# Kernel optimization log

Measured on AMD Instinct MI355X. Metric: run time of the kernel, lower is better.

## Reference

```python
import jax, jax.numpy as jnp
import numpy as np

TOP_K = 2


def setup_inputs() -> dict:
    key = jax.random.key(0)
    ks = jax.random.split(key, 5)
    B, S, D, E, I = 1, 2048, 2880, 8, 2880
    scale_in = 1.0 / np.sqrt(D)
    scale_mid = 1.0 / np.sqrt(I)
    return {
        "x": jax.random.normal(ks[0], (B, S, D), dtype=jnp.float32),
        "w_router": jax.random.normal(ks[1], (D, E), dtype=jnp.float32) * scale_in,
        "w_gate": jax.random.normal(ks[2], (E, D, I), dtype=jnp.float32) * scale_in,
        "w_up": jax.random.normal(ks[3], (E, D, I), dtype=jnp.float32) * scale_in,
        "w_down": jax.random.normal(ks[4], (E, I, D), dtype=jnp.float32) * scale_mid,
    }


def reference(x, w_router, w_gate, w_up, w_down):
    B, S, D = x.shape
    E = w_router.shape[1]
    t = x.reshape(-1, D)  # [T, D] flattened tokens

    # --- RouterTopK: softmax over experts, then top-k selection ---
    logits = t @ w_router                      # [T, E]
    affinities = jax.nn.softmax(logits, axis=-1)
    top_vals, top_idx = jax.lax.top_k(affinities, TOP_K)   # [T, K]
    # normalize_top_k_affinities=True: renormalize selected weights to sum to 1
    top_vals = top_vals / jnp.sum(top_vals, axis=-1, keepdims=True)

    # scatter normalized weights into dense [T, E] combine matrix
    T = t.shape[0]
    tok = jnp.arange(T)[:, None]
    weights = jnp.zeros((T, E), dtype=t.dtype).at[tok, top_idx].set(top_vals)

    # --- Expert SiLU-GLU MLPs (computed per expert, combined by weights) ---
    gate = jnp.einsum("td,edi->eti", t, w_gate)  # [E, T, I]
    up = jnp.einsum("td,edi->eti", t, w_up)      # [E, T, I]
    h = jax.nn.silu(gate) * up                   # [E, T, I]
    y = jnp.einsum("eti,eid->etd", h, w_down)    # [E, T, D]

    out = jnp.einsum("te,etd->td", weights, y)   # affinity-weighted combine
    return out.reshape(B, S, D)
```

## Files before the change

### kernel.cpp

```cpp
#include <hip/hip_runtime.h>
#include <hip/hip_fp16.h>
#include <stdint.h>
#include <math.h>


typedef _Float16 f16;
typedef _Float16 f16x8 __attribute__((ext_vector_type(8)));
typedef float f32x4 __attribute__((ext_vector_type(4)));

#define T_TOK 2048
#define DDIM 2880
#define NEXP 8
#define IDIM 2880
#define BK 64
#define NKT 45

#define BM_A 128
#define BN1_A 96
#define BN2_A 192
#define MAXMT_A 40
#define NB1_A (30*MAXMT_A)
#define NB2_A (15*MAXMT_A)
#define BM_B 256
#define BN1_B 96
#define BN2_B 192
#define MAXMT_B 24
#define NB1_B (30*MAXMT_B)
#define NB2_B (15*MAXMT_B)

#define SLOT_CAP 6144

#define M_COUNT 0
#define M_CUR 8
#define M_OFFS 16
#define M_NTILES 25
#define M_TILE_E 32
#define M_TILE_R0 96
#define M_SLOT_TOK 160
#define M_SLOT_OF (160+SLOT_CAP)
#define M_TOK_E (M_SLOT_OF + 2*T_TOK)
#define META_INTS (M_TOK_E + 2*T_TOK)

#define WT_B   ((size_t)NEXP*DDIM*IDIM*2)
#define A_WGT  ((size_t)0)
#define A_WUT  (A_WGT + WT_B)
#define A_WDT  A_WGT
#define A_HBUF (A_WUT + WT_B)
#define A_YBUF (A_HBUF + (size_t)5120*IDIM*2)
#define A_XH   (A_YBUF + (size_t)5120*DDIM*2)
#define A_META (A_XH + (size_t)T_TOK*DDIM*2)
#define A_SLOTW (A_META + (size_t)META_INTS*4)
#define A_TOKW  (A_SLOTW + (size_t)SLOT_CAP*4)
#define A_NEED  (A_TOKW + (size_t)T_TOK*2*4)

#define B_HBUF ((size_t)0)
#define B_XH   (B_HBUF + (size_t)SLOT_CAP*IDIM*2)
#define B_YBUF B_XH
#define B_META (B_YBUF + (size_t)SLOT_CAP*DDIM*2)
#define B_SLOTW (B_META + (size_t)META_INTS*4)
#define B_TOKW  (B_SLOTW + (size_t)SLOT_CAP*4)
#define B_NEED  (B_TOKW + (size_t)T_TOK*2*4)

__device__ __forceinline__ int swz(int row) { return ((row ^ (row >> 3)) & 7) << 4; }

__device__ __forceinline__ void gload_lds16(const void* gp, void* lp) {
  __builtin_amdgcn_global_load_lds(
      (const __attribute__((address_space(1))) uint32_t*)gp,
      (__attribute__((address_space(3))) uint32_t*)lp,
      16, 0, 0);
}

__global__ __launch_bounds__(256) void k_router(
    const float* __restrict__ x, const float* __restrict__ wr,
    int* __restrict__ meta, float* __restrict__ tok_w) {
  const int lane = threadIdx.x & 63;
  const int t = blockIdx.x * 4 + (threadIdx.x >> 6);
  double acc[NEXP];
#pragma unroll
  for (int e = 0; e < NEXP; e++) acc[e] = 0.0;
  for (int d = lane; d < DDIM; d += 64) {
    float xv = x[(size_t)t * DDIM + d];
    float4 w0 = *(const float4*)(wr + (size_t)d * NEXP);
    float4 w1 = *(const float4*)(wr + (size_t)d * NEXP + 4);
    acc[0] += (double)xv * (double)w0.x;
    acc[1] += (double)xv * (double)w0.y;
    acc[2] += (double)xv * (double)w0.z;
    acc[3] += (double)xv * (double)w0.w;
    acc[4] += (double)xv * (double)w1.x;
    acc[5] += (double)xv * (double)w1.y;
    acc[6] += (double)xv * (double)w1.z;
    acc[7] += (double)xv * (double)w1.w;
  }
#pragma unroll
  for (int m = 32; m >= 1; m >>= 1) {
#pragma unroll
    for (int e = 0; e < NEXP; e++) acc[e] += __shfl_xor(acc[e], m, 64);
  }
  if (lane == 0) {
    int e0 = 0;
#pragma unroll
    for (int e = 1; e < NEXP; e++) if (acc[e] > acc[e0]) e0 = e;
    int e1 = (e0 == 0) ? 1 : 0;
#pragma unroll
    for (int e = 0; e < NEXP; e++) if (e != e0 && acc[e] > acc[e1]) e1 = e;
    double w0 = 1.0 / (1.0 + exp(acc[e1] - acc[e0]));
    meta[M_TOK_E + 2*t]     = e0;
    meta[M_TOK_E + 2*t + 1] = e1;
    tok_w[2*t]     = (float)w0;
    tok_w[2*t + 1] = (float)(1.0 - w0);
    atomicAdd(&meta[M_COUNT + e0], 1);
    atomicAdd(&meta[M_COUNT + e1], 1);
  }
}

__global__ __launch_bounds__(256) void k_xcvt(const float* __restrict__ x, f16* __restrict__ xh) {
  size_t i = ((size_t)blockIdx.x * 256 + threadIdx.x) * 8;
  float4 a = *(const float4*)(x + i);
  float4 b = *(const float4*)(x + i + 4);
  f16x8 v;
  v[0]=(f16)a.x; v[1]=(f16)a.y; v[2]=(f16)a.z; v[3]=(f16)a.w;
  v[4]=(f16)b.x; v[5]=(f16)b.y; v[6]=(f16)b.z; v[7]=(f16)b.w;
  *(f16x8*)(xh + i) = v;
}

__global__ __launch_bounds__(256) void k_cvt_w(const float* __restrict__ src, f16* __restrict__ dst) {
  __shared__ f16 t[64][72];
  const int tile = blockIdx.x;
  const int e = blockIdx.y;
  const int k0 = (tile / 45) * 64;
  const int i0 = (tile % 45) * 64;
  const int tid = threadIdx.x;
  const float* sp = src + ((size_t)e * DDIM + k0) * IDIM + i0;
#pragma unroll
  for (int p = 0; p < 4; p++) {
    int kr = p * 16 + (tid >> 4);
    int c0 = (tid & 15) * 4;
    float4 v = *(const float4*)(sp + (size_t)kr * IDIM + c0);
    t[c0 + 0][kr] = (f16)v.x;
    t[c0 + 1][kr] = (f16)v.y;
    t[c0 + 2][kr] = (f16)v.z;
    t[c0 + 3][kr] = (f16)v.w;
  }
  __syncthreads();
#pragma unroll
  for (int p = 0; p < 2; p++) {
    int row = tid >> 2;
    int ch = (tid & 3) + p * 4;
    f16x8 o = *(const f16x8*)&t[row][ch * 8];
    *(f16x8*)(dst + ((size_t)e * IDIM + i0 + row) * DDIM + k0 + ch * 8) = o;
  }
}

__global__ __launch_bounds__(64) void k_scan(int* __restrict__ meta, float* __restrict__ slot_w, int bm) {
  __shared__ int s_off[NEXP], s_cnt[NEXP], s_pc[NEXP];
  if (threadIdx.x == 0) {
    int run = 0, nt = 0;
    for (int e = 0; e < NEXP; e++) {
      int c = meta[M_COUNT + e];
      int mt = (c + bm - 1) / bm;
      meta[M_OFFS + e] = run;
      s_off[e] = run; s_cnt[e] = c; s_pc[e] = mt * bm;
      for (int j = 0; j < mt; j++) { meta[M_TILE_E + nt] = e; meta[M_TILE_R0 + nt] = run + j * bm; nt++; }
      run += mt * bm;
      meta[M_CUR + e] = 0;
    }
    meta[M_OFFS + NEXP] = run;
    meta[M_NTILES] = nt;
  }
  __syncthreads();
  for (int e = 0; e < NEXP; e++) {
    for (int i = s_cnt[e] + (int)threadIdx.x; i < s_pc[e]; i += 64) {
      meta[M_SLOT_TOK + s_off[e] + i] = 0;
      slot_w[s_off[e] + i] = 0.0f;
    }
  }
}

__global__ __launch_bounds__(256) void k_scatter(int* __restrict__ meta,
    float* __restrict__ slot_w, const float* __restrict__ tok_w) {
  int t = blockIdx.x * 256 + threadIdx.x;
  if (t >= T_TOK) return;
#pragma unroll
  for (int k = 0; k < 2; k++) {
    int e = meta[M_TOK_E + 2*t + k];
    int pos = atomicAdd(&meta[M_CUR + e], 1);
    int slot = meta[M_OFFS + e] + pos;
    meta[M_SLOT_TOK + slot] = t;
    slot_w[slot] = tok_w[2*t + k];
    meta[M_SLOT_OF + 2*t + k] = slot;
  }
}


__global__ __launch_bounds__(256, 3) void kg1(
    const f16* __restrict__ xh, const f16* __restrict__ wgT, const f16* __restrict__ wuT,
    f16* __restrict__ hbuf, const int* __restrict__ meta) {
  const int id = blockIdx.x;
  const int sid = (id & 7) * (NB1_A / 8) + (id >> 3);
  const int mt = sid % MAXMT_A;
  const int nb = sid / MAXMT_A;
  if (mt >= meta[M_NTILES]) return;
  const int e  = meta[M_TILE_E + mt];
  const int r0 = meta[M_TILE_R0 + mt];
  const int n0 = nb * BN1_A;

  __shared__ ushort sA[BM_A * BK];
  __shared__ ushort sBg[BN1_A * BK];
  __shared__ ushort sBu[BN1_A * BK];

  const int tid = threadIdx.x;
  const int lane = tid & 63;
  const int w = tid >> 6;
  const int wm = w >> 1, wn = w & 1;

  const char* aG[4]; int aL[4];
#pragma unroll
  for (int i = 0; i < 4; i++) {
    int seg = w * 4 + i;
    int row = seg * 8 + (lane >> 3);
    int colb = ((lane & 7) * 16) ^ swz(row);
    int tok = meta[M_SLOT_TOK + r0 + row];
    aG[i] = (const char*)(xh + (size_t)tok * DDIM) + colb;
    aL[i] = seg * 1024;
  }
  const char* gG[3]; const char* uG[3]; int bL[3];
#pragma unroll
  for (int i = 0; i < 3; i++) {
    int seg = w * 3 + i;
    int row = seg * 8 + (lane >> 3);
    int colb = ((lane & 7) * 16) ^ swz(row);
    gG[i] = (const char*)(wgT + ((size_t)e * IDIM + n0 + row) * DDIM) + colb;
    uG[i] = (const char*)(wuT + ((size_t)e * IDIM + n0 + row) * DDIM) + colb;
    bL[i] = seg * 1024;
  }

  f32x4 accG[4][3], accU[4][3];
#pragma unroll
  for (int i = 0; i < 4; i++)
#pragma unroll
    for (int j = 0; j < 3; j++) { accG[i][j] = {0.f,0.f,0.f,0.f}; accU[i][j] = {0.f,0.f,0.f,0.f}; }

  for (int kt = 0; kt < NKT; kt++) {
    __syncthreads();
#pragma unroll
    for (int i = 0; i < 4; i++) gload_lds16(aG[i] + kt * 128, (char*)sA + aL[i]);
#pragma unroll
    for (int i = 0; i < 3; i++) gload_lds16(gG[i] + kt * 128, (char*)sBg + bL[i]);
#pragma unroll
    for (int i = 0; i < 3; i++) gload_lds16(uG[i] + kt * 128, (char*)sBu + bL[i]);
    __syncthreads();
#pragma unroll
    for (int kk = 0; kk < 2; kk++) {
      const int gb = kk * 64 + ((lane >> 4) * 16);
      f16x8 af[4], bg[3], bu[3];
#pragma unroll
      for (int fm = 0; fm < 4; fm++) {
        int row = wm * 64 + fm * 16 + (lane & 15);
        af[fm] = *(const f16x8*)((const char*)sA + row * 128 + (gb ^ swz(row)));
      }
#pragma unroll
      for (int fn = 0; fn < 3; fn++) {
        int row = wn * 48 + fn * 16 + (lane & 15);
        bg[fn] = *(const f16x8*)((const char*)sBg + row * 128 + (gb ^ swz(row)));
        bu[fn] = *(const f16x8*)((const char*)sBu + row * 128 + (gb ^ swz(row)));
      }
#pragma unroll
      for (int fm = 0; fm < 4; fm++)
#pragma unroll
        for (int fn = 0; fn < 3; fn++) {
          accG[fm][fn] = __builtin_amdgcn_mfma_f32_16x16x32_f16(af[fm], bg[fn], accG[fm][fn], 0, 0, 0);
          accU[fm][fn] = __builtin_amdgcn_mfma_f32_16x16x32_f16(af[fm], bu[fn], accU[fm][fn], 0, 0, 0);
        }
    }
  }
  const int rl4 = (lane >> 4) * 4;
  const int cl  = lane & 15;
#pragma unroll
  for (int fm = 0; fm < 4; fm++)
#pragma unroll
    for (int fn = 0; fn < 3; fn++)
#pragma unroll
      for (int j = 0; j < 4; j++) {
        int row = wm * 64 + fm * 16 + rl4 + j;
        int col = n0 + wn * 48 + fn * 16 + cl;
        float g = accG[fm][fn][j], u = accU[fm][fn][j];
        float h = g * u / (1.0f + __expf(-g));
        hbuf[(size_t)(r0 + row) * IDIM + col] = (f16)h;
      }
}

__global__ __launch_bounds__(256, 3) void kg2(
    const f16* __restrict__ hbuf, const f16* __restrict__ wdT,
    f16* __restrict__ ybuf, const int* __restrict__ meta, const float* __restrict__ slot_w) {
  const int id = blockIdx.x;
  const int sid = (id & 7) * (NB2_A / 8) + (id >> 3);
  const int mt = sid % MAXMT_A;
  const int nb = sid / MAXMT_A;
  if (mt >= meta[M_NTILES]) return;
  const int e  = meta[M_TILE_E + mt];
  const int r0 = meta[M_TILE_R0 + mt];
  const int n0 = nb * BN2_A;

  __shared__ ushort sA[BM_A * BK];
  __shared__ ushort sB[BN2_A * BK];

  const int tid = threadIdx.x;
  const int lane = tid & 63;
  const int w = tid >> 6;
  const int wm = w >> 1, wn = w & 1;

  const char* aG[4]; int aL[4];
#pragma unroll
  for (int i = 0; i < 4; i++) {
    int seg = w * 4 + i;
    int row = seg * 8 + (lane >> 3);
    int colb = ((lane & 7) * 16) ^ swz(row);
    aG[i] = (const char*)(hbuf + (size_t)(r0 + row) * IDIM) + colb;
    aL[i] = seg * 1024;
  }
  const char* bG[6]; int bL[6];
#pragma unroll
  for (int i = 0; i < 6; i++) {
    int seg = w * 6 + i;
    int row = seg * 8 + (lane >> 3);
    int colb = ((lane & 7) * 16) ^ swz(row);
    bG[i] = (const char*)(wdT + ((size_t)e * DDIM + n0 + row) * IDIM) + colb;
    bL[i] = seg * 1024;
  }

  f32x4 acc[4][6];
#pragma unroll
  for (int i = 0; i < 4; i++)
#pragma unroll
    for (int j = 0; j < 6; j++) acc[i][j] = {0.f,0.f,0.f,0.f};

  for (int kt = 0; kt < NKT; kt++) {
    __syncthreads();
#pragma unroll
    for (int i = 0; i < 4; i++) gload_lds16(aG[i] + kt * 128, (char*)sA + aL[i]);
#pragma unroll
    for (int i = 0; i < 6; i++) gload_lds16(bG[i] + kt * 128, (char*)sB + bL[i]);
    __syncthreads();
#pragma unroll
    for (int kk = 0; kk < 2; kk++) {
      const int gb = kk * 64 + ((lane >> 4) * 16);
      f16x8 af[4], bf[6];
#pragma unroll
      for (int fm = 0; fm < 4; fm++) {
        int row = wm * 64 + fm * 16 + (lane & 15);
        af[fm] = *(const f16x8*)((const char*)sA + row * 128 + (gb ^ swz(row)));
      }
#pragma unroll
      for (int fn = 0; fn < 6; fn++) {
        int row = wn * 96 + fn * 16 + (lane & 15);
        bf[fn] = *(const f16x8*)((const char*)sB + row * 128 + (gb ^ swz(row)));
      }
#pragma unroll
      for (int fm = 0; fm < 4; fm++)
#pragma unroll
        for (int fn = 0; fn < 6; fn++)
          acc[fm][fn] = __builtin_amdgcn_mfma_f32_16x16x32_f16(af[fm], bf[fn], acc[fm][fn], 0, 0, 0);
    }
  }
  const int rl4 = (lane >> 4) * 4;
  const int cl  = lane & 15;
#pragma unroll
  for (int fm = 0; fm < 4; fm++)
#pragma unroll
    for (int j = 0; j < 4; j++) {
      int row = wm * 64 + fm * 16 + rl4 + j;
      int slot = r0 + row;
      float wv = slot_w[slot];
#pragma unroll
      for (int fn = 0; fn < 6; fn++) {
        int col = n0 + wn * 96 + fn * 16 + cl;
        ybuf[(size_t)slot * DDIM + col] = (f16)(acc[fm][fn][j] * wv);
      }
    }
}

__global__ __launch_bounds__(256) void k_combine(const f16* __restrict__ ybuf,
    const int* __restrict__ meta, float* __restrict__ out) {
  size_t idx = (size_t)blockIdx.x * 256 + threadIdx.x;
  int t = (int)(idx / (DDIM/8));
  int c = (int)(idx % (DDIM/8));
  int s0 = meta[M_SLOT_OF + 2*t];
  int s1 = meta[M_SLOT_OF + 2*t + 1];
  f16x8 a = *(const f16x8*)(ybuf + (size_t)s0 * DDIM + c*8);
  f16x8 b = *(const f16x8*)(ybuf + (size_t)s1 * DDIM + c*8);
  float4 o0, o1;
  o0.x = (float)a[0] + (float)b[0];
  o0.y = (float)a[1] + (float)b[1];
  o0.z = (float)a[2] + (float)b[2];
  o0.w = (float)a[3] + (float)b[3];
  o1.x = (float)a[4] + (float)b[4];
  o1.y = (float)a[5] + (float)b[5];
  o1.z = (float)a[6] + (float)b[6];
  o1.w = (float)a[7] + (float)b[7];
  float* op = out + (size_t)t * DDIM + c*8;
  *(float4*)op = o0;
  *(float4*)(op + 4) = o1;
}


__global__ __launch_bounds__(512, 2) void kg1_fb(
    const f16* __restrict__ xh, const float* __restrict__ wg, const float* __restrict__ wu,
    f16* __restrict__ hbuf, const int* __restrict__ meta) {
  const int id = blockIdx.x;
  const int sid = (id & 7) * (NB1_B / 8) + (id >> 3);
  const int mt = sid % MAXMT_B;
  const int nb = sid / MAXMT_B;
  if (mt >= meta[M_NTILES]) return;
  const int e  = meta[M_TILE_E + mt];
  const int r0 = meta[M_TILE_R0 + mt];
  const int n0 = nb * BN1_B;

  __shared__ ushort sA[2][BM_B * BK];
  __shared__ ushort sB[2][2][BN1_B * BK];

  const int tid  = threadIdx.x;
  const int lane = tid & 63;
  const int w    = tid >> 6;
  const int wm   = w >> 1;
  const int gu   = w & 1;

  const char* a_gbase[4];
  int a_loff[4];
#pragma unroll
  for (int i = 0; i < 4; i++) {
    int seg = w * 4 + i;
    int row = seg * 8 + (lane >> 3);
    int colb = ((lane & 7) * 16) ^ swz(row);
    int tok = meta[M_SLOT_TOK + r0 + row];
    a_gbase[i] = (const char*)(xh + (size_t)tok * DDIM) + colb;
    a_loff[i] = seg * 1024;
  }
  const int bm_ = tid / 192;
  const int tt  = tid % 192;
  const int bn0 = (tt % 24) * 4;
  const int bk0 = (tt / 24) * 8;
  const bool bact = tid < 384;
  const float* bsrc = (bm_ ? wu : wg) + ((size_t)e * DDIM + bk0) * IDIM + n0 + bn0;

  float4 vB[8];
  f32x4 acc[4][6];
#pragma unroll
  for (int i = 0; i < 4; i++)
#pragma unroll
    for (int j = 0; j < 6; j++) acc[i][j] = {0.f,0.f,0.f,0.f};

#pragma unroll
  for (int i = 0; i < 4; i++) gload_lds16(a_gbase[i], (char*)sA[0] + a_loff[i]);
  if (bact) {
#pragma unroll
    for (int j = 0; j < 8; j++) vB[j] = *(const float4*)(bsrc + (size_t)j * IDIM);
#pragma unroll
    for (int c = 0; c < 4; c++) {
      f16x8 p;
#pragma unroll
      for (int j = 0; j < 8; j++) {
        float fc = (c==0) ? vB[j].x : (c==1) ? vB[j].y : (c==2) ? vB[j].z : vB[j].w;
        p[j] = (f16)fc;
      }
      *(f16x8*)((char*)sB[0][bm_] + (bn0 + c) * 128 + ((bk0 * 2) ^ swz(bn0 + c))) = p;
    }
  }
  __syncthreads();

  for (int kt = 0; kt < NKT; kt++) {
    const int cur = kt & 1;
    if (kt + 1 < NKT) {
#pragma unroll
      for (int i = 0; i < 4; i++)
        gload_lds16(a_gbase[i] + (kt + 1) * 128, (char*)sA[cur ^ 1] + a_loff[i]);
      if (bact) {
        const float* bs = bsrc + (size_t)(kt + 1) * BK * IDIM;
#pragma unroll
        for (int j = 0; j < 8; j++) vB[j] = *(const float4*)(bs + (size_t)j * IDIM);
      }
    }
#pragma unroll
    for (int kk = 0; kk < 2; kk++) {
      const int gb = kk * 64 + ((lane >> 4) * 16);
      f16x8 af[4], bf[6];
#pragma unroll
      for (int fm = 0; fm < 4; fm++) {
        int row = wm * 64 + fm * 16 + (lane & 15);
        af[fm] = *(const f16x8*)((const char*)sA[cur] + row * 128 + (gb ^ swz(row)));
      }
#pragma unroll
      for (int fn = 0; fn < 6; fn++) {
        int row = fn * 16 + (lane & 15);
        bf[fn] = *(const f16x8*)((const char*)sB[cur][gu] + row * 128 + (gb ^ swz(row)));
      }
#pragma unroll
      for (int fm = 0; fm < 4; fm++)
#pragma unroll
        for (int fn = 0; fn < 6; fn++)
          acc[fm][fn] = __builtin_amdgcn_mfma_f32_16x16x32_f16(af[fm], bf[fn], acc[fm][fn], 0, 0, 0);
    }
    if (kt + 1 < NKT && bact) {
#pragma unroll
      for (int c = 0; c < 4; c++) {
        f16x8 p;
#pragma unroll
        for (int j = 0; j < 8; j++) {
          float fc = (c==0) ? vB[j].x : (c==1) ? vB[j].y : (c==2) ? vB[j].z : vB[j].w;
          p[j] = (f16)fc;
        }
        *(f16x8*)((char*)sB[cur ^ 1][bm_] + (bn0 + c) * 128 + ((bk0 * 2) ^ swz(bn0 + c))) = p;
      }
    }
    __syncthreads();
  }

  float* u_lds = (float*)&sA[0][0];
  const int rl4 = (lane >> 4) * 4;
  const int cl  = lane & 15;
#pragma unroll
  for (int r = 0; r < 2; r++) {
    __syncthreads();
    if (gu == 1) {
#pragma unroll
      for (int fi = 0; fi < 2; fi++)
#pragma unroll
        for (int fn = 0; fn < 6; fn++)
#pragma unroll
          for (int j = 0; j < 4; j++)
            u_lds[wm * 3200 + (fi * 16 + rl4 + j) * 100 + fn * 16 + cl] = acc[2*r + fi][fn][j];
    }
    __syncthreads();
    if (gu == 0) {
#pragma unroll
      for (int fi = 0; fi < 2; fi++) {
        int fm = 2*r + fi;
#pragma unroll
        for (int fn = 0; fn < 6; fn++)
#pragma unroll
          for (int j = 0; j < 4; j++) {
            float u = u_lds[wm * 3200 + (fi * 16 + rl4 + j) * 100 + fn * 16 + cl];
            float g = acc[fm][fn][j];
            float h = g * u / (1.0f + __expf(-g));
            hbuf[(size_t)(r0 + wm * 64 + fm * 16 + rl4 + j) * IDIM + n0 + fn * 16 + cl] = (f16)h;
          }
      }
    }
  }
}

__global__ __launch_bounds__(512, 2) void kg2_fb(
    const f16* __restrict__ hbuf, const float* __restrict__ wd,
    f16* __restrict__ ybuf, const int* __restrict__ meta, const float* __restrict__ slot_w) {
  const int id = blockIdx.x;
  const int sid = (id & 7) * (NB2_B / 8) + (id >> 3);
  const int mt = sid % MAXMT_B;
  const int nb = sid / MAXMT_B;
  if (mt >= meta[M_NTILES]) return;
  const int e  = meta[M_TILE_E + mt];
  const int r0 = meta[M_TILE_R0 + mt];
  const int n0 = nb * BN2_B;

  __shared__ ushort sA[2][BM_B * BK];
  __shared__ ushort sB1[2][BN2_B * BK];

  const int tid  = threadIdx.x;
  const int lane = tid & 63;
  const int w    = tid >> 6;
  const int wm   = w >> 1;
  const int wn   = w & 1;

  const char* a_gbase[4];
  int a_loff[4];
#pragma unroll
  for (int i = 0; i < 4; i++) {
    int seg = w * 4 + i;
    int row = seg * 8 + (lane >> 3);
    int colb = ((lane & 7) * 16) ^ swz(row);
    a_gbase[i] = (const char*)(hbuf + (size_t)(r0 + row) * IDIM) + colb;
    a_loff[i] = seg * 1024;
  }
  const int half = tid / 192;
  const int tt   = tid % 192;
  const int bn0  = half * 96 + (tt % 24) * 4;
  const int bk0  = (tt / 24) * 8;
  const bool bact = tid < 384;
  const float* bsrc = wd + ((size_t)e * IDIM + bk0) * DDIM + n0 + bn0;

  float4 vB[8];
  f32x4 acc[4][6];
#pragma unroll
  for (int i = 0; i < 4; i++)
#pragma unroll
    for (int j = 0; j < 6; j++) acc[i][j] = {0.f,0.f,0.f,0.f};

#pragma unroll
  for (int i = 0; i < 4; i++) gload_lds16(a_gbase[i], (char*)sA[0] + a_loff[i]);
  if (bact) {
#pragma unroll
    for (int j = 0; j < 8; j++) vB[j] = *(const float4*)(bsrc + (size_t)j * DDIM);
#pragma unroll
    for (int c = 0; c < 4; c++) {
      f16x8 p;
#pragma unroll
      for (int j = 0; j < 8; j++) {
        float fc = (c==0) ? vB[j].x : (c==1) ? vB[j].y : (c==2) ? vB[j].z : vB[j].w;
        p[j] = (f16)fc;
      }
      *(f16x8*)((char*)sB1[0] + (bn0 + c) * 128 + ((bk0 * 2) ^ swz(bn0 + c))) = p;
    }
  }
  __syncthreads();

  for (int kt = 0; kt < NKT; kt++) {
    const int cur = kt & 1;
    if (kt + 1 < NKT) {
#pragma unroll
      for (int i = 0; i < 4; i++)
        gload_lds16(a_gbase[i] + (kt + 1) * 128, (char*)sA[cur ^ 1] + a_loff[i]);
      if (bact) {
        const float* bs = bsrc + (size_t)(kt + 1) * BK * DDIM;
#pragma unroll
        for (int j = 0; j < 8; j++) vB[j] = *(const float4*)(bs + (size_t)j * DDIM);
      }
    }
#pragma unroll
    for (int kk = 0; kk < 2; kk++) {
      const int gb = kk * 64 + ((lane >> 4) * 16);
      f16x8 af[4], bf[6];
#pragma unroll
      for (int fm = 0; fm < 4; fm++) {
        int row = wm * 64 + fm * 16 + (lane & 15);
        af[fm] = *(const f16x8*)((const char*)sA[cur] + row * 128 + (gb ^ swz(row)));
      }
#pragma unroll
      for (int fn = 0; fn < 6; fn++) {
        int row = wn * 96 + fn * 16 + (lane & 15);
        bf[fn] = *(const f16x8*)((const char*)sB1[cur] + row * 128 + (gb ^ swz(row)));
      }
#pragma unroll
      for (int fm = 0; fm < 4; fm++)
#pragma unroll
        for (int fn = 0; fn < 6; fn++)
          acc[fm][fn] = __builtin_amdgcn_mfma_f32_16x16x32_f16(af[fm], bf[fn], acc[fm][fn], 0, 0, 0);
    }
    if (kt + 1 < NKT && bact) {
#pragma unroll
      for (int c = 0; c < 4; c++) {
        f16x8 p;
#pragma unroll
        for (int j = 0; j < 8; j++) {
          float fc = (c==0) ? vB[j].x : (c==1) ? vB[j].y : (c==2) ? vB[j].z : vB[j].w;
          p[j] = (f16)fc;
        }
        *(f16x8*)((char*)sB1[cur ^ 1] + (bn0 + c) * 128 + ((bk0 * 2) ^ swz(bn0 + c))) = p;
      }
    }
    __syncthreads();
  }

  const int rl4 = (lane >> 4) * 4;
  const int cl  = lane & 15;
#pragma unroll
  for (int fm = 0; fm < 4; fm++)
#pragma unroll
    for (int j = 0; j < 4; j++) {
      int row = wm * 64 + fm * 16 + rl4 + j;
      int slot = r0 + row;
      float wv = slot_w[slot];
#pragma unroll
      for (int fn = 0; fn < 6; fn++) {
        int col = n0 + wn * 96 + fn * 16 + cl;
        ybuf[(size_t)slot * DDIM + col] = (f16)(acc[fm][fn][j] * wv);
      }
    }
}

extern "C" void kernel_launch(void* const* d_in, const int* in_sizes, int n_in,
                              void* d_out, int out_size, void* d_ws, size_t ws_size,
                              hipStream_t stream) {
  const float* x  = (const float*)d_in[0];
  const float* wr = (const float*)d_in[1];
  const float* wg = (const float*)d_in[2];
  const float* wu = (const float*)d_in[3];
  const float* wd = (const float*)d_in[4];
  float* out = (float*)d_out;
  char* ws = (char*)d_ws;

  if (ws_size >= A_NEED) {
    f16* wgT = (f16*)(ws + A_WGT);
    f16* wuT = (f16*)(ws + A_WUT);
    f16* wdT = (f16*)(ws + A_WDT);
    f16* hbuf = (f16*)(ws + A_HBUF);
    f16* ybuf = (f16*)(ws + A_YBUF);
    f16* xh   = (f16*)(ws + A_XH);
    int* meta = (int*)(ws + A_META);
    float* slot_w = (float*)(ws + A_SLOTW);
    float* tok_w  = (float*)(ws + A_TOKW);

    hipMemsetAsync(meta + M_COUNT, 0, NEXP * sizeof(int), stream);
    k_cvt_w<<<dim3(2025, NEXP), 256, 0, stream>>>(wg, wgT);
    k_cvt_w<<<dim3(2025, NEXP), 256, 0, stream>>>(wu, wuT);
    k_router<<<T_TOK/4, 256, 0, stream>>>(x, wr, meta, tok_w);
    k_xcvt<<<(T_TOK*DDIM/8)/256, 256, 0, stream>>>(x, xh);
    k_scan<<<1, 64, 0, stream>>>(meta, slot_w, BM_A);
    k_scatter<<<(T_TOK + 255)/256, 256, 0, stream>>>(meta, slot_w, tok_w);
    kg1<<<NB1_A, 256, 0, stream>>>(xh, wgT, wuT, hbuf, meta);
    k_cvt_w<<<dim3(2025, NEXP), 256, 0, stream>>>(wd, wdT);
    kg2<<<NB2_A, 256, 0, stream>>>(hbuf, wdT, ybuf, meta, slot_w);
    k_combine<<<(T_TOK*DDIM/8)/256, 256, 0, stream>>>(ybuf, meta, out);
  } else if (ws_size >= B_NEED) {
    f16* hbuf = (f16*)(ws + B_HBUF);
    f16* xh   = (f16*)(ws + B_XH);
    f16* ybuf = (f16*)(ws + B_YBUF);
    int* meta = (int*)(ws + B_META);
    float* slot_w = (float*)(ws + B_SLOTW);
    float* tok_w  = (float*)(ws + B_TOKW);

    hipMemsetAsync(meta + M_COUNT, 0, NEXP * sizeof(int), stream);
    k_router<<<T_TOK/4, 256, 0, stream>>>(x, wr, meta, tok_w);
    k_xcvt<<<(T_TOK*DDIM/8)/256, 256, 0, stream>>>(x, xh);
    k_scan<<<1, 64, 0, stream>>>(meta, slot_w, BM_B);
    k_scatter<<<(T_TOK + 255)/256, 256, 0, stream>>>(meta, slot_w, tok_w);
    kg1_fb<<<NB1_B, 512, 0, stream>>>(xh, wg, wu, hbuf, meta);
    kg2_fb<<<NB2_B, 512, 0, stream>>>(hbuf, wd, ybuf, meta, slot_w);
    k_combine<<<(T_TOK*DDIM/8)/256, 256, 0, stream>>>(ybuf, meta, out);
  }
}
```

Measured before the change: 691.3 us.

## Fuse prep kernels, overlap down-weight conversion with GEMM1, double-buffer LDS tiles

Merges the gate/up weight conversion, router and x conversion into one persistent launch. When the workspace is large enough, it also folds the down-weight transpose into the GEMM1 launch so the conversion blocks run alongside GEMM1 tiles. The scan and scatter steps become a single block that uses shared-memory atomics. Both GEMM kernels switch to double-buffered LDS prefetch with one barrier per k-step, which raises LDS per block to 80KB and lowers the launch-bounds occupancy hint from 3 to 2.

```diff
diff --git a/kernel.cpp b/kernel.cpp
--- a/kernel.cpp
+++ b/kernel.cpp
@@ -21,6 +21,8 @@
 #define MAXMT_A 40
 #define NB1_A (30*MAXMT_A)
 #define NB2_A (15*MAXMT_A)
+#define NCVT 16200
+
 #define BM_B 256
 #define BN1_B 96
 #define BN2_B 192
@@ -31,7 +33,6 @@
 #define SLOT_CAP 6144
 
 #define M_COUNT 0
-#define M_CUR 8
 #define M_OFFS 16
 #define M_NTILES 25
 #define M_TILE_E 32
@@ -42,24 +43,13 @@
 #define META_INTS (M_TOK_E + 2*T_TOK)
 
 #define WT_B   ((size_t)NEXP*DDIM*IDIM*2)
-#define A_WGT  ((size_t)0)
-#define A_WUT  (A_WGT + WT_B)
-#define A_WDT  A_WGT
-#define A_HBUF (A_WUT + WT_B)
-#define A_YBUF (A_HBUF + (size_t)5120*IDIM*2)
-#define A_XH   (A_YBUF + (size_t)5120*DDIM*2)
-#define A_META (A_XH + (size_t)T_TOK*DDIM*2)
-#define A_SLOTW (A_META + (size_t)META_INTS*4)
-#define A_TOKW  (A_SLOTW + (size_t)SLOT_CAP*4)
-#define A_NEED  (A_TOKW + (size_t)T_TOK*2*4)
-
-#define B_HBUF ((size_t)0)
-#define B_XH   (B_HBUF + (size_t)SLOT_CAP*IDIM*2)
-#define B_YBUF B_XH
-#define B_META (B_YBUF + (size_t)SLOT_CAP*DDIM*2)
-#define B_SLOTW (B_META + (size_t)META_INTS*4)
-#define B_TOKW  (B_SLOTW + (size_t)SLOT_CAP*4)
-#define B_NEED  (B_TOKW + (size_t)T_TOK*2*4)
+#define HB_B   ((size_t)5120*IDIM*2)
+#define XH_B   ((size_t)T_TOK*DDIM*2)
+#define TAIL_B ((size_t)META_INTS*4 + (size_t)SLOT_CAP*4 + (size_t)T_TOK*2*4)
+
+#define A3_NEED (3*WT_B + 2*HB_B + XH_B + TAIL_B)
+#define A2_NEED (2*WT_B + 2*HB_B + XH_B + TAIL_B)
+#define BF_NEED ((size_t)SLOT_CAP*IDIM*2 + (size_t)SLOT_CAP*DDIM*2 + TAIL_B)
 
 __device__ __forceinline__ int swz(int row) { return ((row ^ (row >> 3)) & 7) << 4; }
 
@@ -70,11 +60,40 @@
       16, 0, 0);
 }
 
-__global__ __launch_bounds__(256) void k_router(
-    const float* __restrict__ x, const float* __restrict__ wr,
-    int* __restrict__ meta, float* __restrict__ tok_w) {
-  const int lane = threadIdx.x & 63;
-  const int t = blockIdx.x * 4 + (threadIdx.x >> 6);
+
+__device__ __forceinline__ void cvt_body(const float* __restrict__ src, f16* __restrict__ dst,
+                                          int blk, int tid, char* smem) {
+  f16 (*t)[72] = (f16 (*)[72])smem;
+  const int e = blk / 2025;
+  const int tile = blk % 2025;
+  const int k0 = (tile / 45) * 64;
+  const int i0 = (tile % 45) * 64;
+  const float* sp = src + ((size_t)e * DDIM + k0) * IDIM + i0;
+#pragma unroll
+  for (int p = 0; p < 4; p++) {
+    int kr = p * 16 + (tid >> 4);
+    int c0 = (tid & 15) * 4;
+    float4 v = *(const float4*)(sp + (size_t)kr * IDIM + c0);
+    t[c0 + 0][kr] = (f16)v.x;
+    t[c0 + 1][kr] = (f16)v.y;
+    t[c0 + 2][kr] = (f16)v.z;
+    t[c0 + 3][kr] = (f16)v.w;
+  }
+  __syncthreads();
+#pragma unroll
+  for (int p = 0; p < 2; p++) {
+    int row = tid >> 2;
+    int ch = (tid & 3) + p * 4;
+    f16x8 o = *(const f16x8*)&t[row][ch * 8];
+    *(f16x8*)(dst + ((size_t)e * IDIM + i0 + row) * DDIM + k0 + ch * 8) = o;
+  }
+}
+
+__device__ __forceinline__ void router_body(const float* __restrict__ x, const float* __restrict__ wr,
+                                            int* __restrict__ meta, float* __restrict__ tok_w,
+                                            int blk, int tid) {
+  const int lane = tid & 63;
+  const int t = blk * 4 + (tid >> 6);
   double acc[NEXP];
 #pragma unroll
   for (int e = 0; e < NEXP; e++) acc[e] = 0.0;
@@ -113,8 +132,9 @@
   }
 }
 
-__global__ __launch_bounds__(256) void k_xcvt(const float* __restrict__ x, f16* __restrict__ xh) {
-  size_t i = ((size_t)blockIdx.x * 256 + threadIdx.x) * 8;
+__device__ __forceinline__ void xcvt_body(const float* __restrict__ x, f16* __restrict__ xh,
+                                          int blk, int tid) {
+  size_t i = ((size_t)blk * 256 + tid) * 8;
   float4 a = *(const float4*)(x + i);
   float4 b = *(const float4*)(x + i + 4);
   f16x8 v;
@@ -123,79 +143,74 @@
   *(f16x8*)(xh + i) = v;
 }
 
-__global__ __launch_bounds__(256) void k_cvt_w(const float* __restrict__ src, f16* __restrict__ dst) {
-  __shared__ f16 t[64][72];
-  const int tile = blockIdx.x;
-  const int e = blockIdx.y;
-  const int k0 = (tile / 45) * 64;
-  const int i0 = (tile % 45) * 64;
+__global__ __launch_bounds__(256) void k_p1(
+    const float* __restrict__ x, const float* __restrict__ wr,
+    const float* __restrict__ wg, const float* __restrict__ wu,
+    f16* __restrict__ wgT, f16* __restrict__ wuT, f16* __restrict__ xh,
+    int* __restrict__ meta, float* __restrict__ tok_w) {
+  __shared__ char smem[9216];
+  int b = blockIdx.x;
   const int tid = threadIdx.x;
-  const float* sp = src + ((size_t)e * DDIM + k0) * IDIM + i0;
-#pragma unroll
-  for (int p = 0; p < 4; p++) {
-    int kr = p * 16 + (tid >> 4);
-    int c0 = (tid & 15) * 4;
-    float4 v = *(const float4*)(sp + (size_t)kr * IDIM + c0);
-    t[c0 + 0][kr] = (f16)v.x;
-    t[c0 + 1][kr] = (f16)v.y;
-    t[c0 + 2][kr] = (f16)v.z;
-    t[c0 + 3][kr] = (f16)v.w;
-  }
-  __syncthreads();
-#pragma unroll
-  for (int p = 0; p < 2; p++) {
-    int row = tid >> 2;
-    int ch = (tid & 3) + p * 4;
-    f16x8 o = *(const f16x8*)&t[row][ch * 8];
-    *(f16x8*)(dst + ((size_t)e * IDIM + i0 + row) * DDIM + k0 + ch * 8) = o;
-  }
-}
-
-__global__ __launch_bounds__(64) void k_scan(int* __restrict__ meta, float* __restrict__ slot_w, int bm) {
-  __shared__ int s_off[NEXP], s_cnt[NEXP], s_pc[NEXP];
-  if (threadIdx.x == 0) {
+  if (b < NCVT) { cvt_body(wg, wgT, b, tid, smem); return; }
+  b -= NCVT;
+  if (b < NCVT) { cvt_body(wu, wuT, b, tid, smem); return; }
+  b -= NCVT;
+  if (b < T_TOK/4) { router_body(x, wr, meta, tok_w, b, tid); return; }
+  b -= T_TOK/4;
+  xcvt_body(x, xh, b, tid);
+}
+
+__global__ __launch_bounds__(256) void k_router(const float* x, const float* wr, int* meta, float* tok_w) {
+  router_body(x, wr, meta, tok_w, blockIdx.x, threadIdx.x);
+}
+__global__ __launch_bounds__(256) void k_xcvt(const float* x, f16* xh) {
+  xcvt_body(x, xh, blockIdx.x, threadIdx.x);
+}
+__global__ __launch_bounds__(256) void k_cvt_w(const float* src, f16* dst) {
+  __shared__ char smem[9216];
+  cvt_body(src, dst, blockIdx.x, threadIdx.x, smem);
+}
+
+__global__ __launch_bounds__(256) void k_scan_scatter(
+    int* __restrict__ meta, float* __restrict__ slot_w, const float* __restrict__ tok_w, int bm) {
+  __shared__ int s_off[NEXP], s_cnt[NEXP], s_pc[NEXP], s_cur[NEXP];
+  const int tid = threadIdx.x;
+  if (tid == 0) {
     int run = 0, nt = 0;
     for (int e = 0; e < NEXP; e++) {
       int c = meta[M_COUNT + e];
       int mt = (c + bm - 1) / bm;
       meta[M_OFFS + e] = run;
-      s_off[e] = run; s_cnt[e] = c; s_pc[e] = mt * bm;
+      s_off[e] = run; s_cnt[e] = c; s_pc[e] = mt * bm; s_cur[e] = 0;
       for (int j = 0; j < mt; j++) { meta[M_TILE_E + nt] = e; meta[M_TILE_R0 + nt] = run + j * bm; nt++; }
       run += mt * bm;
-      meta[M_CUR + e] = 0;
     }
     meta[M_OFFS + NEXP] = run;
     meta[M_NTILES] = nt;
   }
   __syncthreads();
   for (int e = 0; e < NEXP; e++) {
-    for (int i = s_cnt[e] + (int)threadIdx.x; i < s_pc[e]; i += 64) {
+    for (int i = s_cnt[e] + tid; i < s_pc[e]; i += 256) {
       meta[M_SLOT_TOK + s_off[e] + i] = 0;
       slot_w[s_off[e] + i] = 0.0f;
     }
   }
-}
-
-__global__ __launch_bounds__(256) void k_scatter(int* __restrict__ meta,
-    float* __restrict__ slot_w, const float* __restrict__ tok_w) {
-  int t = blockIdx.x * 256 + threadIdx.x;
-  if (t >= T_TOK) return;
-#pragma unroll
-  for (int k = 0; k < 2; k++) {
-    int e = meta[M_TOK_E + 2*t + k];
-    int pos = atomicAdd(&meta[M_CUR + e], 1);
-    int slot = meta[M_OFFS + e] + pos;
-    meta[M_SLOT_TOK + slot] = t;
-    slot_w[slot] = tok_w[2*t + k];
-    meta[M_SLOT_OF + 2*t + k] = slot;
-  }
-}
-
-
-__global__ __launch_bounds__(256, 3) void kg1(
+  for (int t = tid; t < T_TOK; t += 256) {
+#pragma unroll
+    for (int k = 0; k < 2; k++) {
+      int e = meta[M_TOK_E + 2*t + k];
+      int pos = atomicAdd(&s_cur[e], 1);
+      int slot = s_off[e] + pos;
+      meta[M_SLOT_TOK + slot] = t;
+      slot_w[slot] = tok_w[2*t + k];
+      meta[M_SLOT_OF + 2*t + k] = slot;
+    }
+  }
+}
+
+__device__ __forceinline__ void kg1_body(
     const f16* __restrict__ xh, const f16* __restrict__ wgT, const f16* __restrict__ wuT,
-    f16* __restrict__ hbuf, const int* __restrict__ meta) {
-  const int id = blockIdx.x;
+    f16* __restrict__ hbuf, const int* __restrict__ meta, int id, int tid, char* smem) {
   const int sid = (id & 7) * (NB1_A / 8) + (id >> 3);
   const int mt = sid % MAXMT_A;
   const int nb = sid / MAXMT_A;
@@ -204,11 +219,6 @@
   const int r0 = meta[M_TILE_R0 + mt];
   const int n0 = nb * BN1_A;
 
-  __shared__ ushort sA[BM_A * BK];
-  __shared__ ushort sBg[BN1_A * BK];
-  __shared__ ushort sBu[BN1_A * BK];
-
-  const int tid = threadIdx.x;
   const int lane = tid & 63;
   const int w = tid >> 6;
   const int wm = w >> 1, wn = w & 1;
@@ -240,15 +250,31 @@
 #pragma unroll
     for (int j = 0; j < 3; j++) { accG[i][j] = {0.f,0.f,0.f,0.f}; accU[i][j] = {0.f,0.f,0.f,0.f}; }
 
+#pragma unroll
+  for (int i = 0; i < 4; i++) gload_lds16(aG[i], smem + aL[i]);
+#pragma unroll
+  for (int i = 0; i < 3; i++) gload_lds16(gG[i], smem + 32768 + bL[i]);
+#pragma unroll
+  for (int i = 0; i < 3; i++) gload_lds16(uG[i], smem + 57344 + bL[i]);
+  __syncthreads();
+
   for (int kt = 0; kt < NKT; kt++) {
-    __syncthreads();
-#pragma unroll
-    for (int i = 0; i < 4; i++) gload_lds16(aG[i] + kt * 128, (char*)sA + aL[i]);
-#pragma unroll
-    for (int i = 0; i < 3; i++) gload_lds16(gG[i] + kt * 128, (char*)sBg + bL[i]);
-#pragma unroll
-    for (int i = 0; i < 3; i++) gload_lds16(uG[i] + kt * 128, (char*)sBu + bL[i]);
-    __syncthreads();
+    const int cur = kt & 1;
+    char* curA  = smem + cur * 16384;
+    char* curBg = smem + 32768 + cur * 12288;
+    char* curBu = smem + 57344 + cur * 12288;
+    if (kt + 1 < NKT) {
+      const int nx = cur ^ 1;
+      char* nxA  = smem + nx * 16384;
+      char* nxBg = smem + 32768 + nx * 12288;
+      char* nxBu = smem + 57344 + nx * 12288;
+#pragma unroll
+      for (int i = 0; i < 4; i++) gload_lds16(aG[i] + (kt+1) * 128, nxA + aL[i]);
+#pragma unroll
+      for (int i = 0; i < 3; i++) gload_lds16(gG[i] + (kt+1) * 128, nxBg + bL[i]);
+#pragma unroll
+      for (int i = 0; i < 3; i++) gload_lds16(uG[i] + (kt+1) * 128, nxBu + bL[i]);
+    }
 #pragma unroll
     for (int kk = 0; kk < 2; kk++) {
       const int gb = kk * 64 + ((lane >> 4) * 16);
@@ -256,13 +282,13 @@
 #pragma unroll
       for (int fm = 0; fm < 4; fm++) {
         int row = wm * 64 + fm * 16 + (lane & 15);
-        af[fm] = *(const f16x8*)((const char*)sA + row * 128 + (gb ^ swz(row)));
+        af[fm] = *(const f16x8*)(curA + row * 128 + (gb ^ swz(row)));
       }
 #pragma unroll
       for (int fn = 0; fn < 3; fn++) {
         int row = wn * 48 + fn * 16 + (lane & 15);
-        bg[fn] = *(const f16x8*)((const char*)sBg + row * 128 + (gb ^ swz(row)));
-        bu[fn] = *(const f16x8*)((const char*)sBu + row * 128 + (gb ^ swz(row)));
+        bg[fn] = *(const f16x8*)(curBg + row * 128 + (gb ^ swz(row)));
+        bu[fn] = *(const f16x8*)(curBu + row * 128 + (gb ^ swz(row)));
       }
 #pragma unroll
       for (int fm = 0; fm < 4; fm++)
@@ -272,7 +298,9 @@
           accU[fm][fn] = __builtin_amdgcn_mfma_f32_16x16x32_f16(af[fm], bu[fn], accU[fm][fn], 0, 0, 0);
         }
     }
-  }
+    __syncthreads();
+  }
+
   const int rl4 = (lane >> 4) * 4;
   const int cl  = lane & 15;
 #pragma unroll
@@ -289,9 +317,20 @@
       }
 }
 
-__global__ __launch_bounds__(256, 3) void kg2(
+__global__ __launch_bounds__(256, 2) void k_g1cvt(
+    const f16* __restrict__ xh, const f16* __restrict__ wgT, const f16* __restrict__ wuT,
+    f16* __restrict__ hbuf, const int* __restrict__ meta,
+    const float* __restrict__ wd, f16* __restrict__ wdT) {
+  __shared__ char smem[81920];
+  const int id = blockIdx.x;
+  if (id < NB1_A) kg1_body(xh, wgT, wuT, hbuf, meta, id, threadIdx.x, smem);
+  else            cvt_body(wd, wdT, id - NB1_A, threadIdx.x, smem);
+}
+
+__global__ __launch_bounds__(256, 2) void kg2(
     const f16* __restrict__ hbuf, const f16* __restrict__ wdT,
     f16* __restrict__ ybuf, const int* __restrict__ meta, const float* __restrict__ slot_w) {
+  __shared__ char smem[81920];
   const int id = blockIdx.x;
   const int sid = (id & 7) * (NB2_A / 8) + (id >> 3);
   const int mt = sid % MAXMT_A;
@@ -301,9 +340,6 @@
   const int r0 = meta[M_TILE_R0 + mt];
   const int n0 = nb * BN2_A;
 
-  __shared__ ushort sA[BM_A * BK];
-  __shared__ ushort sB[BN2_A * BK];
-
   const int tid = threadIdx.x;
   const int lane = tid & 63;
   const int w = tid >> 6;
@@ -334,13 +370,25 @@
 #pragma unroll
     for (int j = 0; j < 6; j++) acc[i][j] = {0.f,0.f,0.f,0.f};
 
+#pragma unroll
+  for (int i = 0; i < 4; i++) gload_lds16(aG[i], smem + aL[i]);
+#pragma unroll
+  for (int i = 0; i < 6; i++) gload_lds16(bG[i], smem + 32768 + bL[i]);
+  __syncthreads();
+
   for (int kt = 0; kt < NKT; kt++) {
-    __syncthreads();
-#pragma unroll
-    for (int i = 0; i < 4; i++) gload_lds16(aG[i] + kt * 128, (char*)sA + aL[i]);
-#pragma unroll
-    for (int i = 0; i < 6; i++) gload_lds16(bG[i] + kt * 128, (char*)sB + bL[i]);
-    __syncthreads();
+    const int cur = kt & 1;
+    char* curA = smem + cur * 16384;
+    char* curB = smem + 32768 + cur * 24576;
+    if (kt + 1 < NKT) {
+      const int nx = cur ^ 1;
+      char* nxA = smem + nx * 16384;
+      char* nxB = smem + 32768 + nx * 24576;
+#pragma unroll
+      for (int i = 0; i < 4; i++) gload_lds16(aG[i] + (kt+1) * 128, nxA + aL[i]);
+#pragma unroll
+      for (int i = 0; i < 6; i++) gload_lds16(bG[i] + (kt+1) * 128, nxB + bL[i]);
+    }
 #pragma unroll
     for (int kk = 0; kk < 2; kk++) {
       const int gb = kk * 64 + ((lane >> 4) * 16);
@@ -348,12 +396,12 @@
 #pragma unroll
       for (int fm = 0; fm < 4; fm++) {
         int row = wm * 64 + fm * 16 + (lane & 15);
-        af[fm] = *(const f16x8*)((const char*)sA + row * 128 + (gb ^ swz(row)));
+        af[fm] = *(const f16x8*)(curA + row * 128 + (gb ^ swz(row)));
       }
 #pragma unroll
       for (int fn = 0; fn < 6; fn++) {
         int row = wn * 96 + fn * 16 + (lane & 15);
-        bf[fn] = *(const f16x8*)((const char*)sB + row * 128 + (gb ^ swz(row)));
+        bf[fn] = *(const f16x8*)(curB + row * 128 + (gb ^ swz(row)));
       }
 #pragma unroll
       for (int fm = 0; fm < 4; fm++)
@@ -361,6 +409,7 @@
         for (int fn = 0; fn < 6; fn++)
           acc[fm][fn] = __builtin_amdgcn_mfma_f32_16x16x32_f16(af[fm], bf[fn], acc[fm][fn], 0, 0, 0);
     }
+    __syncthreads();
   }
   const int rl4 = (lane >> 4) * 4;
   const int cl  = lane & 15;
@@ -686,41 +735,42 @@
   float* out = (float*)d_out;
   char* ws = (char*)d_ws;
 
-  if (ws_size >= A_NEED) {
-    f16* wgT = (f16*)(ws + A_WGT);
-    f16* wuT = (f16*)(ws + A_WUT);
-    f16* wdT = (f16*)(ws + A_WDT);
-    f16* hbuf = (f16*)(ws + A_HBUF);
-    f16* ybuf = (f16*)(ws + A_YBUF);
-    f16* xh   = (f16*)(ws + A_XH);
-    int* meta = (int*)(ws + A_META);
-    float* slot_w = (float*)(ws + A_SLOTW);
-    float* tok_w  = (float*)(ws + A_TOKW);
-
-    hipMemsetAsync(meta + M_COUNT, 0, NEXP * sizeof(int), stream);
-    k_cvt_w<<<dim3(2025, NEXP), 256, 0, stream>>>(wg, wgT);
-    k_cvt_w<<<dim3(2025, NEXP), 256, 0, stream>>>(wu, wuT);
+  if (ws_size >= A2_NEED) {
+    const bool three = (ws_size >= A3_NEED);
+    f16* wgT = (f16*)(ws);
+    f16* wuT = (f16*)(ws + WT_B);
+    f16* wdT = three ? (f16*)(ws + 2*WT_B) : wgT;
+    char* base = ws + (three ? 3*WT_B : 2*WT_B);
+    f16* hbuf = (f16*)(base);
+    f16* ybuf = (f16*)(base + HB_B);
+    f16* xh   = (f16*)(base + 2*HB_B);
+    int* meta = (int*)(base + 2*HB_B + XH_B);
+    float* slot_w = (float*)((char*)meta + META_INTS*4);
+    float* tok_w  = (float*)((char*)slot_w + SLOT_CAP*4);
+
+    (void)hipMemsetAsync(meta + M_COUNT, 0, NEXP * sizeof(int), stream);
+    k_p1<<<2*NCVT + T_TOK/4 + 2880, 256, 0, stream>>>(x, wr, wg, wu, wgT, wuT, xh, meta, tok_w);
+    k_scan_scatter<<<1, 256, 0, stream>>>(meta, slot_w, tok_w, BM_A);
+    if (three) {
+      k_g1cvt<<<NB1_A + NCVT, 256, 0, stream>>>(xh, wgT, wuT, hbuf, meta, wd, wdT);
+    } else {
+      k_g1cvt<<<NB1_A, 256, 0, stream>>>(xh, wgT, wuT, hbuf, meta, wd, wdT);
+      k_cvt_w<<<NCVT, 256, 0, stream>>>(wd, wdT);
+    }
+    kg2<<<NB2_A, 256, 0, stream>>>(hbuf, wdT, ybuf, meta, slot_w);
+    k_combine<<<(T_TOK*DDIM/8)/256, 256, 0, stream>>>(ybuf, meta, out);
+  } else if (ws_size >= BF_NEED) {
+    f16* hbuf = (f16*)(ws);
+    f16* xh   = (f16*)(ws + (size_t)SLOT_CAP*IDIM*2);
+    f16* ybuf = xh;
+    int* meta = (int*)(ws + (size_t)SLOT_CAP*IDIM*2 + (size_t)SLOT_CAP*DDIM*2);
+    float* slot_w = (float*)((char*)meta + META_INTS*4);
+    float* tok_w  = (float*)((char*)slot_w + SLOT_CAP*4);
+
+    (void)hipMemsetAsync(meta + M_COUNT, 0, NEXP * sizeof(int), stream);
     k_router<<<T_TOK/4, 256, 0, stream>>>(x, wr, meta, tok_w);
     k_xcvt<<<(T_TOK*DDIM/8)/256, 256, 0, stream>>>(x, xh);
-    k_scan<<<1, 64, 0, stream>>>(meta, slot_w, BM_A);
-    k_scatter<<<(T_TOK + 255)/256, 256, 0, stream>>>(meta, slot_w, tok_w);
-    kg1<<<NB1_A, 256, 0, stream>>>(xh, wgT, wuT, hbuf, meta);
-    k_cvt_w<<<dim3(2025, NEXP), 256, 0, stream>>>(wd, wdT);
-    kg2<<<NB2_A, 256, 0, stream>>>(hbuf, wdT, ybuf, meta, slot_w);
-    k_combine<<<(T_TOK*DDIM/8)/256, 256, 0, stream>>>(ybuf, meta, out);
-  } else if (ws_size >= B_NEED) {
-    f16* hbuf = (f16*)(ws + B_HBUF);
-    f16* xh   = (f16*)(ws + B_XH);
-    f16* ybuf = (f16*)(ws + B_YBUF);
-    int* meta = (int*)(ws + B_META);
-    float* slot_w = (float*)(ws + B_SLOTW);
-    float* tok_w  = (float*)(ws + B_TOKW);
-
-    hipMemsetAsync(meta + M_COUNT, 0, NEXP * sizeof(int), stream);
-    k_router<<<T_TOK/4, 256, 0, stream>>>(x, wr, meta, tok_w);
-    k_xcvt<<<(T_TOK*DDIM/8)/256, 256, 0, stream>>>(x, xh);
-    k_scan<<<1, 64, 0, stream>>>(meta, slot_w, BM_B);
-    k_scatter<<<(T_TOK + 255)/256, 256, 0, stream>>>(meta, slot_w, tok_w);
+    k_scan_scatter<<<1, 256, 0, stream>>>(meta, slot_w, tok_w, BM_B);
     kg1_fb<<<NB1_B, 512, 0, stream>>>(xh, wg, wu, hbuf, meta);
     kg2_fb<<<NB2_B, 512, 0, stream>>>(hbuf, wd, ybuf, meta, slot_w);
     k_combine<<<(T_TOK*DDIM/8)/256, 256, 0, stream>>>(ybuf, meta, out);
```

After: 580.9 us. 1.19x faster.
